# Kernel optimization log

Hardware: AMD Instinct MI355X
Metric: run time of the kernel (lower is better)

Reference implementation:

```python
import jax, jax.numpy as jnp
import numpy as np

CE_W, BOUND_W, DICE_W, SMOOTH = 1.0, 0.1, 1.0, 1e-6


def setup_inputs() -> dict:
    key = jax.random.key(0)
    k1, k2 = jax.random.split(key)
    B, C, H, W = 8, 1, 256, 256
    logits = jax.random.normal(k1, (B, C, H, W), dtype=jnp.float32)
    target = jax.random.uniform(k2, (B, C, H, W), dtype=jnp.float32)
    return {"logits": logits, "target": target}


def _edt(fg):
    # fg: [B, H, W] bool foreground mask. Returns exact Euclidean distance
    # transform of the background (0 at foreground), matching
    # scipy.ndimage.distance_transform_edt(1 - fg).
    B, H, W = fg.shape
    INF = jnp.float32(H + W)  # larger than any in-image 1D distance

    # --- pass 1: vertical distance to nearest foreground in each column ---
    fg_t = jnp.transpose(fg, (1, 0, 2))  # [H, B, W], scan over rows

    def step(carry, fg_row):
        d = jnp.where(fg_row, 0.0, carry + 1.0)
        return d, d

    init = jnp.full((B, W), INF, dtype=jnp.float32)
    _, g_fwd = jax.lax.scan(step, init, fg_t)                 # top-down
    _, g_bwd = jax.lax.scan(step, init, fg_t, reverse=True)   # bottom-up
    g = jnp.minimum(g_fwd, g_bwd)          # [H, B, W]
    g = jnp.transpose(g, (1, 0, 2))        # [B, H, W]

    # --- pass 2: exact squared EDT per row: min_k (j-k)^2 + g[i,k]^2 ---
    j = jnp.arange(W, dtype=jnp.float32)
    offs2 = (j[:, None] - j[None, :]) ** 2                    # [W, W]
    # [B, H, Wj, Wk] intermediate -> min over k
    dt2 = jnp.min(g[:, :, None, :] ** 2 + offs2[None, None, :, :], axis=-1)
    dt = jnp.sqrt(dt2)

    # empty masks get an all-zero distance map (scipy branch in the original)
    nonempty = jnp.any(fg, axis=(1, 2))
    return jnp.where(nonempty[:, None, None], dt, 0.0)


def reference(logits, target):
    target = jnp.clip(target.astype(jnp.float32), 0.0, 1.0)

    # BCEWithLogitsLoss (mean): stable log(1 + e^x) - x*t
    ce = jnp.mean(jnp.logaddexp(0.0, logits) - logits * target)

    probs = jnp.clip(jax.nn.sigmoid(logits), SMOOTH, 1.0 - SMOOTH)

    # Dice over flattened tensors
    p, t = probs.reshape(-1), target.reshape(-1)
    inter = jnp.sum(p * t)
    dice = 1.0 - (2.0 * inter + SMOOTH) / (jnp.sum(p) + jnp.sum(t) + SMOOTH)

    # Boundary: mean(probs * EDT(target > 0.5)) -- EDT is non-differentiable data
    fg = target[:, 0] > 0.5                      # [B, H, W]
    dt = jax.lax.stop_gradient(_edt(fg))[:, None]  # [B, 1, H, W]
    boundary = jnp.mean(probs * dt)

    total = CE_W * ce + DICE_W * dice + BOUND_W * boundary
    return total, ce, dice, boundary
```

## Files before the change

kernel.cpp:

```cpp
#include <hip/hip_runtime.h>

#define BB 8
#define HH 256
#define WW 256
#define NTOT (BB * HH * WW)
#define RPB 4
#define NBLK (BB * HH / RPB)

__global__ __launch_bounds__(256) void build_masks(
    const float* __restrict__ target, unsigned* __restrict__ masks) {
  const int s = blockIdx.x;
  const int b = blockIdx.y;
  const int j = threadIdx.x;
  const float* base = target + b * (HH * WW) + s * 32 * WW + j;
  unsigned m = 0;
#pragma unroll
  for (int r = 0; r < 32; ++r)
    if (base[r * WW] > 0.5f) m |= (1u << r);
  masks[b * 2048 + s * 256 + j] = m;
}

__global__ __launch_bounds__(256) void main_kernel(
    const float* __restrict__ logits, const float* __restrict__ target,
    const unsigned* __restrict__ masks,
    float* __restrict__ partials ) {
  __shared__ float s_g2[RPB][3 * WW];
  __shared__ float s_red[4 * 5];
  __shared__ int s_im[4 * 2];

  const int g = blockIdx.x;
  const int b = g >> 6;
  const int i0 = (g & 63) * RPB;
  const int j = threadIdx.x;
  const int lane = j & 63, wave = j >> 6;

  unsigned m[8];
#pragma unroll
  for (int w = 0; w < 8; ++w) m[w] = masks[b * 2048 + w * 256 + j];
  const unsigned many = m[0] | m[1] | m[2] | m[3] | m[4] | m[5] | m[6] | m[7];

  int rmax = 0;
#pragma unroll
  for (int r = 0; r < RPB; ++r) {
    const int i = i0 + r;
    const int wi = i >> 5, rr = i & 31;
    int dUp = 1 << 30, dDn = 1 << 30;
    const unsigned cur = m[wi] >> rr;
    if (cur) {
      dUp = __builtin_ctz(cur);
    } else {
      int off = 32 - rr;
      for (int w2 = wi + 1; w2 < 8; ++w2, off += 32)
        if (m[w2]) { dUp = off + __builtin_ctz(m[w2]); break; }
    }
    const unsigned curd = m[wi] << (31 - rr);
    if (curd) {
      dDn = __builtin_clz(curd);
    } else {
      int off = rr + 1;
      for (int w2 = wi - 1; w2 >= 0; --w2, off += 32)
        if (m[w2]) { dDn = off + __builtin_clz(m[w2]); break; }
    }
    const int d = min(dUp, dDn);
    s_g2[r][WW + j] = (d < 256) ? (float)(d * d) : 1.0e9f;
    s_g2[r][j] = 1.0e9f;
    s_g2[r][2 * WW + j] = 1.0e9f;
    rmax = max(rmax, min(d, 255));
  }

  const int wave_any = __any(many != 0u);
#pragma unroll
  for (int off = 32; off > 0; off >>= 1)
    rmax = max(rmax, __shfl_down(rmax, off, 64));
  if (lane == 0) { s_im[wave * 2] = wave_any; s_im[wave * 2 + 1] = rmax; }
  __syncthreads();
  const int nonempty = s_im[0] | s_im[2] | s_im[4] | s_im[6];
  const int R = max(max(s_im[1], s_im[3]), max(s_im[5], s_im[7]));

  float v0 = 0.f, v1 = 0.f, v2 = 0.f, v3 = 0.f, v4 = 0.f;
#pragma unroll
  for (int r = 0; r < RPB; ++r) {
    const float* gp = &s_g2[r][WW + j];
    float mn = gp[0];
    for (int dlt = 1; dlt <= R; ++dlt) {
      const float d2 = (float)(dlt * dlt);
      mn = fminf(mn, fminf(d2 + gp[dlt], d2 + gp[-dlt]));
    }
    const float dt = nonempty ? sqrtf(mn) : 0.0f;

    const int idx = (b * HH + i0 + r) * WW + j;
    const float x = logits[idx];
    float t = target[idx];
    t = fminf(fmaxf(t, 0.0f), 1.0f);
    const float e = __expf(-fabsf(x));
    const float inv = 1.0f / (1.0f + e);
    const float ce = fmaxf(x, 0.0f) + __logf(1.0f + e) - x * t;
    float p = (x >= 0.0f) ? inv : e * inv;
    p = fminf(fmaxf(p, 1e-6f), 1.0f - 1e-6f);
    v0 += ce; v1 += p; v2 += t; v3 += p * t; v4 += p * dt;
  }

  float v[5] = {v0, v1, v2, v3, v4};
#pragma unroll
  for (int q = 0; q < 5; ++q) {
    float s = v[q];
#pragma unroll
    for (int off = 32; off > 0; off >>= 1) s += __shfl_down(s, off, 64);
    if (lane == 0) s_red[wave * 5 + q] = s;
  }
  __syncthreads();
  if (j == 0) {
#pragma unroll
    for (int q = 0; q < 5; ++q)
      partials[q * NBLK + g] =
          s_red[q] + s_red[5 + q] + s_red[10 + q] + s_red[15 + q];
  }
}

__global__ __launch_bounds__(256) void finalize(
    const float* __restrict__ partials, float* __restrict__ out) {
  __shared__ double s_red[4 * 5];
  const int j = threadIdx.x;
  const int lane = j & 63, wave = j >> 6;
  double acc[5];
#pragma unroll
  for (int q = 0; q < 5; ++q)
    acc[q] = (double)partials[q * NBLK + j] +
             (double)partials[q * NBLK + 256 + j];
#pragma unroll
  for (int q = 0; q < 5; ++q) {
    double s = acc[q];
#pragma unroll
    for (int off = 32; off > 0; off >>= 1) s += __shfl_down(s, off, 64);
    if (lane == 0) s_red[wave * 5 + q] = s;
  }
  __syncthreads();
  if (j == 0) {
    double sum[5];
#pragma unroll
    for (int q = 0; q < 5; ++q)
      sum[q] = s_red[q] + s_red[5 + q] + s_red[10 + q] + s_red[15 + q];
    const double n = (double)NTOT;
    const double ce = sum[0] / n;
    const double dice = 1.0 - (2.0 * sum[3] + 1e-6) / (sum[1] + sum[2] + 1e-6);
    const double boundary = sum[4] / n;
    out[0] = (float)(ce + dice + 0.1 * boundary);
    out[1] = (float)ce;
    out[2] = (float)dice;
    out[3] = (float)boundary;
  }
}

extern "C" void kernel_launch(void* const* d_in, const int* in_sizes, int n_in,
                              void* d_out, int out_size, void* d_ws,
                              size_t ws_size, hipStream_t stream) {
  const float* logits = (const float*)d_in[0];
  const float* target = (const float*)d_in[1];
  float* out = (float*)d_out;

  char* ws = (char*)d_ws;
  unsigned* masks = (unsigned*)ws;
  float* partials = (float*)(ws + 64 * 1024);

  build_masks<<<dim3(8, 8), 256, 0, stream>>>(target, masks);
  main_kernel<<<NBLK, 256, 0, stream>>>(logits, target, masks, partials);
  finalize<<<1, 256, 0, stream>>>(partials, out);
}
```

Baseline: 66.29 us.

## Fuse mask building into main kernel and double rows per block

Removes the separate build_masks launch: each block now rebuilds the full per-column foreground bitmasks for its batch image straight from target, reading all 256 rows per column. Rows per block go from 4 to 8, halving the block count to 256, and logits/target for the block's rows are prefetched into registers. Partial sums are still written at 4-row granularity so finalize keeps its layout. This drops one kernel launch and the mask round trip through global memory, but each block re-reads the whole 256KB target image, so redundant target traffic is multiplied (served mostly from L2), and register pressure rises.

```diff
diff --git a/kernel.cpp b/kernel.cpp
--- a/kernel.cpp
+++ b/kernel.cpp
@@ -4,39 +4,45 @@
 #define HH 256
 #define WW 256
 #define NTOT (BB * HH * WW)
-#define RPB 4
+#define RPB 8
 #define NBLK (BB * HH / RPB)
+#define NPART (BB * HH / 4)
 
-__global__ __launch_bounds__(256) void build_masks(
-    const float* __restrict__ target, unsigned* __restrict__ masks) {
-  const int s = blockIdx.x;
-  const int b = blockIdx.y;
-  const int j = threadIdx.x;
-  const float* base = target + b * (HH * WW) + s * 32 * WW + j;
-  unsigned m = 0;
-#pragma unroll
-  for (int r = 0; r < 32; ++r)
-    if (base[r * WW] > 0.5f) m |= (1u << r);
-  masks[b * 2048 + s * 256 + j] = m;
-}
-
-__global__ __launch_bounds__(256) void main_kernel(
+__global__ __launch_bounds__(256) void fused_kernel(
     const float* __restrict__ logits, const float* __restrict__ target,
-    const unsigned* __restrict__ masks,
     float* __restrict__ partials ) {
   __shared__ float s_g2[RPB][3 * WW];
-  __shared__ float s_red[4 * 5];
+  __shared__ float s_red[4][10];
   __shared__ int s_im[4 * 2];
 
   const int g = blockIdx.x;
-  const int b = g >> 6;
-  const int i0 = (g & 63) * RPB;
+  const int b = g >> 5;
+  const int t = g & 31;
+  const int i0 = t * RPB;
   const int j = threadIdx.x;
   const int lane = j & 63, wave = j >> 6;
 
+  const float* tcol = target + b * (HH * WW) + j;
+  const float* lcol = logits + b * (HH * WW) + j;
+
+  float xr[RPB], tr[RPB];
+#pragma unroll
+  for (int r = 0; r < RPB; ++r) {
+    xr[r] = lcol[(i0 + r) * WW];
+    tr[r] = tcol[(i0 + r) * WW];
+  }
+
   unsigned m[8];
 #pragma unroll
-  for (int w = 0; w < 8; ++w) m[w] = masks[b * 2048 + w * 256 + j];
+  for (int w = 0; w < 8; ++w) {
+    float v[32];
+#pragma unroll
+    for (int r = 0; r < 32; ++r) v[r] = tcol[(w * 32 + r) * WW];
+    unsigned mm = 0u;
+#pragma unroll
+    for (int r = 0; r < 32; ++r) mm |= (v[r] > 0.5f) ? (1u << r) : 0u;
+    m[w] = mm;
+  }
   const unsigned many = m[0] | m[1] | m[2] | m[3] | m[4] | m[5] | m[6] | m[7];
 
   int rmax = 0;
@@ -77,7 +83,8 @@
   const int nonempty = s_im[0] | s_im[2] | s_im[4] | s_im[6];
   const int R = max(max(s_im[1], s_im[3]), max(s_im[5], s_im[7]));
 
-  float v0 = 0.f, v1 = 0.f, v2 = 0.f, v3 = 0.f, v4 = 0.f;
+  float va[5] = {0.f, 0.f, 0.f, 0.f, 0.f};
+  float vb[5] = {0.f, 0.f, 0.f, 0.f, 0.f};
 #pragma unroll
   for (int r = 0; r < RPB; ++r) {
     const float* gp = &s_g2[r][WW + j];
@@ -88,32 +95,37 @@
     }
     const float dt = nonempty ? sqrtf(mn) : 0.0f;
 
-    const int idx = (b * HH + i0 + r) * WW + j;
-    const float x = logits[idx];
-    float t = target[idx];
-    t = fminf(fmaxf(t, 0.0f), 1.0f);
+    const float x = xr[r];
+    float tt = tr[r];
+    tt = fminf(fmaxf(tt, 0.0f), 1.0f);
     const float e = __expf(-fabsf(x));
     const float inv = 1.0f / (1.0f + e);
-    const float ce = fmaxf(x, 0.0f) + __logf(1.0f + e) - x * t;
+    const float ce = fmaxf(x, 0.0f) + __logf(1.0f + e) - x * tt;
     float p = (x >= 0.0f) ? inv : e * inv;
     p = fminf(fmaxf(p, 1e-6f), 1.0f - 1e-6f);
-    v0 += ce; v1 += p; v2 += t; v3 += p * t; v4 += p * dt;
+    float* vv = (r < 4) ? va : vb;
+    vv[0] += ce; vv[1] += p; vv[2] += tt; vv[3] += p * tt; vv[4] += p * dt;
   }
 
-  float v[5] = {v0, v1, v2, v3, v4};
+  float v10[10] = {va[0], va[1], va[2], va[3], va[4],
+                   vb[0], vb[1], vb[2], vb[3], vb[4]};
 #pragma unroll
-  for (int q = 0; q < 5; ++q) {
-    float s = v[q];
+  for (int q = 0; q < 10; ++q) {
+    float s = v10[q];
 #pragma unroll
     for (int off = 32; off > 0; off >>= 1) s += __shfl_down(s, off, 64);
-    if (lane == 0) s_red[wave * 5 + q] = s;
+    if (lane == 0) s_red[wave][q] = s;
   }
   __syncthreads();
   if (j == 0) {
+    const int o0 = b * 64 + 2 * t;
 #pragma unroll
-    for (int q = 0; q < 5; ++q)
-      partials[q * NBLK + g] =
-          s_red[q] + s_red[5 + q] + s_red[10 + q] + s_red[15 + q];
+    for (int q = 0; q < 5; ++q) {
+      partials[q * NPART + o0] =
+          s_red[0][q] + s_red[1][q] + s_red[2][q] + s_red[3][q];
+      partials[q * NPART + o0 + 1] =
+          s_red[0][5 + q] + s_red[1][5 + q] + s_red[2][5 + q] + s_red[3][5 + q];
+    }
   }
 }
 
@@ -125,8 +137,8 @@
   double acc[5];
 #pragma unroll
   for (int q = 0; q < 5; ++q)
-    acc[q] = (double)partials[q * NBLK + j] +
-             (double)partials[q * NBLK + 256 + j];
+    acc[q] = (double)partials[q * NPART + j] +
+             (double)partials[q * NPART + 256 + j];
 #pragma unroll
   for (int q = 0; q < 5; ++q) {
     double s = acc[q];
@@ -158,11 +170,8 @@
   const float* target = (const float*)d_in[1];
   float* out = (float*)d_out;
 
-  char* ws = (char*)d_ws;
-  unsigned* masks = (unsigned*)ws;
-  float* partials = (float*)(ws + 64 * 1024);
+  float* partials = (float*)d_ws;
 
-  build_masks<<<dim3(8, 8), 256, 0, stream>>>(target, masks);
-  main_kernel<<<NBLK, 256, 0, stream>>>(logits, target, masks, partials);
+  fused_kernel<<<NBLK, 256, 0, stream>>>(logits, target, partials);
   finalize<<<1, 256, 0, stream>>>(partials, out);
 }
```

After: 73.63 us. +11.1%, slower.

## Fuse mask building into main kernel using per-block halo window scan

Applied to the files above, without the earlier changes.

Removes the separate build_masks kernel. Each block now reads a 36-row window of target around its rows straight from global memory and packs it into a 64-bit mask. When no foreground lies in that window, the column is scanned linearly up or down. Logits and target are also preloaded into registers. This saves one kernel launch and the mask round trip, at the cost of redundant overlapping target reads across blocks and possibly long serial scans when foreground is sparse.

```diff
diff --git a/kernel.cpp b/kernel.cpp
--- a/kernel.cpp
+++ b/kernel.cpp
@@ -6,23 +6,11 @@
 #define NTOT (BB * HH * WW)
 #define RPB 4
 #define NBLK (BB * HH / RPB)
+#define HALO 16
+#define WLEN (RPB + 2 * HALO)
 
-__global__ __launch_bounds__(256) void build_masks(
-    const float* __restrict__ target, unsigned* __restrict__ masks) {
-  const int s = blockIdx.x;
-  const int b = blockIdx.y;
-  const int j = threadIdx.x;
-  const float* base = target + b * (HH * WW) + s * 32 * WW + j;
-  unsigned m = 0;
-#pragma unroll
-  for (int r = 0; r < 32; ++r)
-    if (base[r * WW] > 0.5f) m |= (1u << r);
-  masks[b * 2048 + s * 256 + j] = m;
-}
-
-__global__ __launch_bounds__(256) void main_kernel(
+__global__ __launch_bounds__(256) void fused_kernel(
     const float* __restrict__ logits, const float* __restrict__ target,
-    const unsigned* __restrict__ masks,
     float* __restrict__ partials ) {
   __shared__ float s_g2[RPB][3 * WW];
   __shared__ float s_red[4 * 5];
@@ -34,33 +22,48 @@
   const int j = threadIdx.x;
   const int lane = j & 63, wave = j >> 6;
 
-  unsigned m[8];
+  const float* tcol = target + b * (HH * WW) + j;
+  const float* lcol = logits + b * (HH * WW) + j;
+
+  float xr[RPB], tr[RPB];
 #pragma unroll
-  for (int w = 0; w < 8; ++w) m[w] = masks[b * 2048 + w * 256 + j];
-  const unsigned many = m[0] | m[1] | m[2] | m[3] | m[4] | m[5] | m[6] | m[7];
+  for (int r = 0; r < RPB; ++r) {
+    xr[r] = lcol[(i0 + r) * WW];
+    tr[r] = tcol[(i0 + r) * WW];
+  }
+
+  const int base = i0 - HALO;
+  unsigned long long w64 = 0ull;
+#pragma unroll
+  for (int k = 0; k < WLEN; ++k) {
+    const int row = base + k;
+    const int rc = min(max(row, 0), HH - 1);
+    const float v = tcol[rc * WW];
+    if (row >= 0 && row < HH && v > 0.5f) w64 |= (1ull << k);
+  }
+
+  int fgDown = 1 << 20;
+  int fgUp = -(1 << 20);
+  if ((w64 >> (RPB - 1 + HALO)) == 0ull) {
+    for (int row = i0 + RPB - 1 + HALO + 1; row < HH; ++row)
+      if (tcol[row * WW] > 0.5f) { fgDown = row; break; }
+  }
+  if ((w64 << (63 - HALO)) == 0ull) {
+    for (int row = i0 - HALO - 1; row >= 0; --row)
+      if (tcol[row * WW] > 0.5f) { fgUp = row; break; }
+  }
+  const bool found =
+      (w64 != 0ull) || (fgDown < (1 << 19)) || (fgUp > -(1 << 19));
 
   int rmax = 0;
 #pragma unroll
   for (int r = 0; r < RPB; ++r) {
     const int i = i0 + r;
-    const int wi = i >> 5, rr = i & 31;
-    int dUp = 1 << 30, dDn = 1 << 30;
-    const unsigned cur = m[wi] >> rr;
-    if (cur) {
-      dUp = __builtin_ctz(cur);
-    } else {
-      int off = 32 - rr;
-      for (int w2 = wi + 1; w2 < 8; ++w2, off += 32)
-        if (m[w2]) { dUp = off + __builtin_ctz(m[w2]); break; }
-    }
-    const unsigned curd = m[wi] << (31 - rr);
-    if (curd) {
-      dDn = __builtin_clz(curd);
-    } else {
-      int off = rr + 1;
-      for (int w2 = wi - 1; w2 >= 0; --w2, off += 32)
-        if (m[w2]) { dDn = off + __builtin_clz(m[w2]); break; }
-    }
+    const int p = r + HALO;
+    const unsigned long long bd = w64 >> p;
+    const unsigned long long bu = w64 << (63 - p);
+    const int dUp = bd ? __builtin_ctzll(bd) : (fgDown - i);
+    const int dDn = bu ? __builtin_clzll(bu) : (i - fgUp);
     const int d = min(dUp, dDn);
     s_g2[r][WW + j] = (d < 256) ? (float)(d * d) : 1.0e9f;
     s_g2[r][j] = 1.0e9f;
@@ -68,7 +71,7 @@
     rmax = max(rmax, min(d, 255));
   }
 
-  const int wave_any = __any(many != 0u);
+  const int wave_any = __any(found);
 #pragma unroll
   for (int off = 32; off > 0; off >>= 1)
     rmax = max(rmax, __shfl_down(rmax, off, 64));
@@ -88,9 +91,8 @@
     }
     const float dt = nonempty ? sqrtf(mn) : 0.0f;
 
-    const int idx = (b * HH + i0 + r) * WW + j;
-    const float x = logits[idx];
-    float t = target[idx];
+    const float x = xr[r];
+    float t = tr[r];
     t = fminf(fmaxf(t, 0.0f), 1.0f);
     const float e = __expf(-fabsf(x));
     const float inv = 1.0f / (1.0f + e);
@@ -158,11 +160,8 @@
   const float* target = (const float*)d_in[1];
   float* out = (float*)d_out;
 
-  char* ws = (char*)d_ws;
-  unsigned* masks = (unsigned*)ws;
-  float* partials = (float*)(ws + 64 * 1024);
+  float* partials = (float*)d_ws;
 
-  build_masks<<<dim3(8, 8), 256, 0, stream>>>(target, masks);
-  main_kernel<<<NBLK, 256, 0, stream>>>(logits, target, masks, partials);
+  fused_kernel<<<NBLK, 256, 0, stream>>>(logits, target, partials);
   finalize<<<1, 256, 0, stream>>>(partials, out);
 }
```

Measured after the change: 67.77 us. 2.2% more time.
